# Kernel tuning notes

Measured on AMD Instinct MI355X. Metric: run time of the kernel, lower is better.

Reference implementation:

```python
import jax, jax.numpy as jnp
import numpy as np

B, S, HS, HHS, NH = 128, 8000, 9, 8, 4
HD = HHS // NH  # head dim = 2


def _layernorm(x, g, b, eps=1e-6):
    m = jnp.mean(x, axis=-1, keepdims=True)
    v = jnp.mean((x - m) ** 2, axis=-1, keepdims=True)
    return (x - m) * jax.lax.rsqrt(v + eps) * g + b


def _binding(a, b):
    # HRR binding: circular convolution along last dim
    return jnp.fft.ifft(jnp.fft.fft(a) * jnp.fft.fft(b)).real


def _unbinding(s, a):
    # HRR unbinding: circular correlation along last dim
    return jnp.fft.ifft(jnp.fft.fft(s) * jnp.conj(jnp.fft.fft(a))).real


def _cosine_sim(a, b, eps=1e-8):
    num = jnp.sum(a * b, axis=-1, keepdims=True)
    na = jnp.maximum(jnp.linalg.norm(a, axis=-1, keepdims=True), eps)
    nb = jnp.maximum(jnp.linalg.norm(b, axis=-1, keepdims=True), eps)
    return num / (na * nb)


def _heads(x):  # [B,S,HHS] -> [B,NH,S,HD]
    return x.reshape(B, S, NH, HD).transpose(0, 2, 1, 3)


def setup_inputs() -> dict:
    key = jax.random.key(0)
    ks = jax.random.split(key, 12)
    p = {}
    p["x"] = jax.random.normal(ks[0], (B, S, HS), dtype=jnp.float32)
    p["mask"] = jnp.ones((B, NH, S, 1), dtype=jnp.float32)
    p["pos_bias"] = jax.random.normal(ks[1], (1, S, HS), dtype=jnp.float32) * 0.02
    p["ln_g"] = jnp.ones((HS,), dtype=jnp.float32)
    p["ln_b"] = jnp.zeros((HS,), dtype=jnp.float32)
    p["Wq"] = jax.random.normal(ks[2], (HHS, HS), dtype=jnp.float32) * 0.3
    p["bq"] = jnp.zeros((HHS,), dtype=jnp.float32)
    p["Wk"] = jax.random.normal(ks[3], (HHS, HS), dtype=jnp.float32) * 0.3
    p["bk"] = jnp.zeros((HHS,), dtype=jnp.float32)
    p["Wv"] = jax.random.normal(ks[4], (HHS, HS), dtype=jnp.float32) * 0.3
    p["bv"] = jnp.zeros((HHS,), dtype=jnp.float32)
    p["W1"] = jax.random.normal(ks[5], (HS, HHS), dtype=jnp.float32) * 0.3
    p["b1"] = jnp.zeros((HS,), dtype=jnp.float32)
    p["W2"] = jax.random.normal(ks[6], (HS, HHS), dtype=jnp.float32) * 0.3
    p["b2"] = jnp.zeros((HS,), dtype=jnp.float32)
    p["Wo"] = jax.random.normal(ks[7], (1, HS), dtype=jnp.float32) * 0.3
    p["bo"] = jnp.zeros((1,), dtype=jnp.float32)
    return p


def reference(x, mask, pos_bias, ln_g, ln_b, Wq, bq, Wk, bk, Wv, bv, W1, b1, W2, b2, Wo, bo):
    x = x + pos_bias
    x = _layernorm(x, ln_g, ln_b)
    q = _heads(x @ Wq.T + bq)  # [B,NH,S,HD]
    k = _heads(x @ Wk.T + bk)
    v = _heads(x @ Wv.T + bv)
    bind = _binding(k, v).sum(axis=-2, keepdims=True)  # [B,NH,1,HD]
    vp = _unbinding(bind, q)                            # [B,NH,S,HD]
    scale = _cosine_sim(v, vp)                          # [B,NH,S,1]
    scale = scale + (1.0 - mask) * -1e9
    weight = jax.nn.softmax(scale, axis=-2)             # softmax over S
    weighted = weight * v                               # [B,NH,S,HD]
    attn_out = weighted.transpose(0, 2, 1, 3).reshape(B, S, HHS)
    # NOTE: original has dead code h=ffn1(attn_out); h=layernorm(h+x)
    # which is immediately overwritten and does not affect the output.
    h = jax.nn.gelu(attn_out @ W2.T + b2, approximate=False) + x
    return h @ Wo.T + bo  # [B,S,1]
```

## Files before the change

### kernel.cpp

```cpp
#include <hip/hip_runtime.h>
#include <math.h>

#define TB 256
#define S_LEN 8000
#define B_N 128
#define BPB 8
#define TPB 4
#define GRID (B_N * BPB)
#define CTRW 32


__device__ __forceinline__ void matvec89(const float* __restrict__ W, const float* __restrict__ bias,
                                         const float* __restrict__ y, float* out) {
#pragma unroll
  for (int i = 0; i < 8; ++i) {
    float a = bias[i];
#pragma unroll
    for (int j = 0; j < 9; ++j) a += W[i * 9 + j] * y[j];
    out[i] = a;
  }
}

__device__ __forceinline__ float head_scale(const float* q, const float* v, const float* bindS,
                                            int h, float maskv) {
  float q0 = q[2 * h], q1 = q[2 * h + 1];
  float v0 = v[2 * h], v1 = v[2 * h + 1];
  float B0 = bindS[2 * h], B1 = bindS[2 * h + 1];
  float vp0 = B0 * q0 + B1 * q1;
  float vp1 = B0 * q1 + B1 * q0;
  float num = v0 * vp0 + v1 * vp1;
  float a2 = fmaxf(v0 * v0 + v1 * v1, 1e-16f);
  float b2 = fmaxf(vp0 * vp0 + vp1 * vp1, 1e-16f);
  float sc = num * rsqrtf(a2 * b2);
  sc += (1.f - maskv) * (-1e9f);
  return sc;
}

__device__ __forceinline__ void batch_barrier(unsigned* ctr, int tid) {
  __syncthreads();
  if (tid == 0) {
    __hip_atomic_fetch_add(ctr, 1u, __ATOMIC_RELAXED, __HIP_MEMORY_SCOPE_AGENT);
    while (__hip_atomic_load(ctr, __ATOMIC_RELAXED, __HIP_MEMORY_SCOPE_AGENT) < (unsigned)BPB)
      __builtin_amdgcn_s_sleep(8);
  }
  __syncthreads();
}

__global__ void k_init(unsigned* __restrict__ ctrs, float* __restrict__ gws,
                       const float* __restrict__ W2, const float* __restrict__ b2,
                       const float* __restrict__ Wo, const float* __restrict__ bo) {
  int tid = blockIdx.x * blockDim.x + threadIdx.x;
  if (tid < 2 * B_N * CTRW) ctrs[tid] = 0u;
  if (blockIdx.x == 0 && threadIdx.x == 0) {
    float G[8];
#pragma unroll
    for (int j = 0; j < 8; ++j) G[j] = 0.f;
    float C0 = bo[0];
#pragma unroll
    for (int i = 0; i < 9; ++i) {
      float b = b2[i];
      float Phi = 0.5f * (1.f + erff(b * 0.70710678118654752f));
      float phi = 0.39894228040143268f * __expf(-0.5f * b * b);
      C0 += Wo[i] * (b * Phi);
      float wg = Wo[i] * (Phi + b * phi);
#pragma unroll
      for (int j = 0; j < 8; ++j) G[j] += wg * W2[i * 8 + j];
    }
#pragma unroll
    for (int j = 0; j < 8; ++j) gws[j] = G[j];
    gws[8] = C0;
  }
}

__global__ __launch_bounds__(TB, 4) void k_fused(
    const float* __restrict__ x, const float* __restrict__ mask, const float* __restrict__ pos,
    const float* __restrict__ lng, const float* __restrict__ lnb,
    const float* __restrict__ Wq, const float* __restrict__ bq,
    const float* __restrict__ Wk, const float* __restrict__ bk,
    const float* __restrict__ Wv, const float* __restrict__ bv,
    const float* __restrict__ Wo,
    const float* __restrict__ gws,
    unsigned* __restrict__ ctr1, unsigned* __restrict__ ctr2,
    float* __restrict__ bindP, float* __restrict__ sumP,
    float* __restrict__ out) {
  __shared__ float red[4 * 8];
  __shared__ float sib[BPB * 8];
  __shared__ float bindS[8], invDS[4];

  const int tid = threadIdx.x, bid = blockIdx.x;
  const int b = bid >> 3;
  const int t0 = (bid & 7) * TPB;
  const int wave = tid >> 6, lane = tid & 63;
  const float* maskb = mask + (size_t)b * 4 * S_LEN;

  int nrowA[TPB];
#pragma unroll
  for (int t = 0; t < TPB; ++t) nrowA[t] = min(TB, S_LEN - (t0 + t) * TB);

  float y[TPB][9];
  float vv[TPB][8];
  float acc[8];
#pragma unroll
  for (int i = 0; i < 8; ++i) acc[i] = 0.f;

#pragma unroll
  for (int t = 0; t < TPB; ++t) {
    if (tid < nrowA[t]) {
      const int s = (t0 + t) * TB + tid;
      const float* xr = x + ((size_t)b * S_LEN + s) * 9;
      const float* pr = pos + (size_t)s * 9;
      float m = 0.f;
#pragma unroll
      for (int j = 0; j < 9; ++j) { y[t][j] = xr[j] + pr[j]; m += y[t][j]; }
      m *= (1.f / 9.f);
      float var = 0.f;
#pragma unroll
      for (int j = 0; j < 9; ++j) { float d = y[t][j] - m; var += d * d; }
      var *= (1.f / 9.f);
      float rs = rsqrtf(var + 1e-6f);
#pragma unroll
      for (int j = 0; j < 9; ++j) y[t][j] = (y[t][j] - m) * rs * lng[j] + lnb[j];

      float kk[8];
      matvec89(Wk, bk, y[t], kk);
      matvec89(Wv, bv, y[t], vv[t]);
#pragma unroll
      for (int h = 0; h < 4; ++h) {
        float k0 = kk[2 * h], k1 = kk[2 * h + 1];
        float v0 = vv[t][2 * h], v1 = vv[t][2 * h + 1];
        acc[2 * h]     += k0 * v0 + k1 * v1;
        acc[2 * h + 1] += k0 * v1 + k1 * v0;
      }
    }
  }
#pragma unroll
  for (int i = 0; i < 8; ++i) {
#pragma unroll
    for (int off = 32; off > 0; off >>= 1) acc[i] += __shfl_down(acc[i], off, 64);
  }
  __syncthreads();
  if (lane == 0) {
#pragma unroll
    for (int i = 0; i < 8; ++i) red[wave * 8 + i] = acc[i];
  }
  __syncthreads();
  if (tid < 8) {
    float s = red[tid] + red[8 + tid] + red[16 + tid] + red[24 + tid];
    __hip_atomic_store(&bindP[bid * 8 + tid], s, __ATOMIC_RELAXED, __HIP_MEMORY_SCOPE_AGENT);
  }

  batch_barrier(&ctr1[b * CTRW], tid);

  if (tid < BPB * 8)
    sib[tid] = __hip_atomic_load(&bindP[(size_t)b * BPB * 8 + tid],
                                 __ATOMIC_RELAXED, __HIP_MEMORY_SCOPE_AGENT);
  __syncthreads();
  if (tid < 8) {
    float s = 0.f;
#pragma unroll
    for (int j = 0; j < BPB; ++j) s += sib[j * 8 + tid];
    bindS[tid] = s;
  }
  __syncthreads();

  float e[TPB][4];
  float gv[TPB][4];
  float oy[TPB];
  float esum[4] = {0.f, 0.f, 0.f, 0.f};
#pragma unroll
  for (int t = 0; t < TPB; ++t) {
    const int s0 = (t0 + t) * TB;
#pragma unroll
    for (int h = 0; h < 4; ++h) { e[t][h] = 0.f; gv[t][h] = 0.f; }
    oy[t] = 0.f;
    if (tid < nrowA[t]) {
      float qq[8];
      matvec89(Wq, bq, y[t], qq);
#pragma unroll
      for (int h = 0; h < 4; ++h) {
        float m = maskb[(size_t)h * S_LEN + s0 + tid];
        e[t][h] = __expf(head_scale(qq, vv[t], bindS, h, m));
        esum[h] += e[t][h];
        gv[t][h] = gws[2 * h] * vv[t][2 * h] + gws[2 * h + 1] * vv[t][2 * h + 1];
      }
      float o = 0.f;
#pragma unroll
      for (int i = 0; i < 9; ++i) o += Wo[i] * y[t][i];
      oy[t] = o;
    }
  }
#pragma unroll
  for (int h = 0; h < 4; ++h) {
#pragma unroll
    for (int off = 32; off > 0; off >>= 1) esum[h] += __shfl_down(esum[h], off, 64);
  }
  __syncthreads();
  if (lane == 0) {
#pragma unroll
    for (int h = 0; h < 4; ++h) red[wave * 4 + h] = esum[h];
  }
  __syncthreads();
  if (tid < 4) {
    float s = red[tid] + red[4 + tid] + red[8 + tid] + red[12 + tid];
    __hip_atomic_store(&sumP[bid * 4 + tid], s, __ATOMIC_RELAXED, __HIP_MEMORY_SCOPE_AGENT);
  }

  batch_barrier(&ctr2[b * CTRW], tid);

  if (tid < BPB * 4)
    sib[tid] = __hip_atomic_load(&sumP[(size_t)b * BPB * 4 + tid],
                                 __ATOMIC_RELAXED, __HIP_MEMORY_SCOPE_AGENT);
  __syncthreads();
  if (tid < 4) {
    float s = 0.f;
#pragma unroll
    for (int j = 0; j < BPB; ++j) s += sib[j * 4 + tid];
    invDS[tid] = 1.f / s;
  }
  __syncthreads();

  const float C0 = gws[8];
#pragma unroll
  for (int t = 0; t < TPB; ++t) {
    const int s0 = (t0 + t) * TB;
    if (tid < nrowA[t]) {
      float o = C0 + oy[t];
#pragma unroll
      for (int h = 0; h < 4; ++h) o += (e[t][h] * invDS[h]) * gv[t][h];
      out[(size_t)b * S_LEN + s0 + tid] = o;
    }
  }
}


extern "C" void kernel_launch(void* const* d_in, const int* in_sizes, int n_in,
                              void* d_out, int out_size, void* d_ws, size_t ws_size,
                              hipStream_t stream) {
  const float* x    = (const float*)d_in[0];
  const float* mask = (const float*)d_in[1];
  const float* pos  = (const float*)d_in[2];
  const float* lng  = (const float*)d_in[3];
  const float* lnb  = (const float*)d_in[4];
  const float* Wq   = (const float*)d_in[5];
  const float* bq   = (const float*)d_in[6];
  const float* Wk   = (const float*)d_in[7];
  const float* bk   = (const float*)d_in[8];
  const float* Wv   = (const float*)d_in[9];
  const float* bv   = (const float*)d_in[10];
  const float* W2   = (const float*)d_in[13];
  const float* b2   = (const float*)d_in[14];
  const float* Wo   = (const float*)d_in[15];
  const float* bo   = (const float*)d_in[16];
  float* out = (float*)d_out;

  unsigned* ctr1  = (unsigned*)d_ws;
  unsigned* ctr2  = ctr1 + B_N * CTRW;
  float*    gws   = (float*)(ctr2 + B_N * CTRW);
  float*    bindP = gws + 16;
  float*    sumP  = bindP + GRID * 8;

  k_init<<<(2 * B_N * CTRW + 255) / 256, 256, 0, stream>>>(ctr1, gws, W2, b2, Wo, bo);
  k_fused<<<GRID, TB, 0, stream>>>(x, mask, pos, lng, lnb, Wq, bq, Wk, bk, Wv, bv,
                                   Wo, gws, ctr1, ctr2, bindP, sumP, out);
}
```

Baseline: 32.08 us.

## Split first batch barrier into arrive/wait and overlap Q projection and mask loads

The first cross-block barrier becomes separate arrive and wait phases. Between them each block loads its mask values and computes the Q projection, the output projection term and the gate-weighted V term, so this work overlaps with waiting for the other blocks of the same batch. The spin-wait sleep interval also drops from 8 to 1. Keeping qq, mm and related values live across the barrier raises register pressure, which could reduce occupancy under the 4-blocks-per-SM launch bound.

```diff
diff --git a/kernel.cpp b/kernel.cpp
--- a/kernel.cpp
+++ b/kernel.cpp
@@ -41,7 +41,19 @@
   if (tid == 0) {
     __hip_atomic_fetch_add(ctr, 1u, __ATOMIC_RELAXED, __HIP_MEMORY_SCOPE_AGENT);
     while (__hip_atomic_load(ctr, __ATOMIC_RELAXED, __HIP_MEMORY_SCOPE_AGENT) < (unsigned)BPB)
-      __builtin_amdgcn_s_sleep(8);
+      __builtin_amdgcn_s_sleep(1);
+  }
+  __syncthreads();
+}
+__device__ __forceinline__ void barrier_arrive(unsigned* ctr, int tid) {
+  __syncthreads();
+  if (tid == 0)
+    __hip_atomic_fetch_add(ctr, 1u, __ATOMIC_RELAXED, __HIP_MEMORY_SCOPE_AGENT);
+}
+__device__ __forceinline__ void barrier_wait(unsigned* ctr, int tid) {
+  if (tid == 0) {
+    while (__hip_atomic_load(ctr, __ATOMIC_RELAXED, __HIP_MEMORY_SCOPE_AGENT) < (unsigned)BPB)
+      __builtin_amdgcn_s_sleep(1);
   }
   __syncthreads();
 }
@@ -149,7 +161,38 @@
     __hip_atomic_store(&bindP[bid * 8 + tid], s, __ATOMIC_RELAXED, __HIP_MEMORY_SCOPE_AGENT);
   }
 
-  batch_barrier(&ctr1[b * CTRW], tid);
+  barrier_arrive(&ctr1[b * CTRW], tid);
+
+  float mm[TPB][4];
+#pragma unroll
+  for (int t = 0; t < TPB; ++t) {
+    const int s = (t0 + t) * TB + tid;
+    if (tid < nrowA[t]) {
+#pragma unroll
+      for (int h = 0; h < 4; ++h) mm[t][h] = maskb[(size_t)h * S_LEN + s];
+    }
+  }
+  float qq[TPB][8];
+  float gv[TPB][4];
+  float oy[TPB];
+#pragma unroll
+  for (int t = 0; t < TPB; ++t) {
+#pragma unroll
+    for (int h = 0; h < 4; ++h) gv[t][h] = 0.f;
+    oy[t] = 0.f;
+    if (tid < nrowA[t]) {
+      matvec89(Wq, bq, y[t], qq[t]);
+      float o = 0.f;
+#pragma unroll
+      for (int i = 0; i < 9; ++i) o += Wo[i] * y[t][i];
+      oy[t] = o;
+#pragma unroll
+      for (int h = 0; h < 4; ++h)
+        gv[t][h] = gws[2 * h] * vv[t][2 * h] + gws[2 * h + 1] * vv[t][2 * h + 1];
+    }
+  }
+
+  barrier_wait(&ctr1[b * CTRW], tid);
 
   if (tid < BPB * 8)
     sib[tid] = __hip_atomic_load(&bindP[(size_t)b * BPB * 8 + tid],
@@ -164,29 +207,17 @@
   __syncthreads();
 
   float e[TPB][4];
-  float gv[TPB][4];
-  float oy[TPB];
   float esum[4] = {0.f, 0.f, 0.f, 0.f};
 #pragma unroll
   for (int t = 0; t < TPB; ++t) {
-    const int s0 = (t0 + t) * TB;
-#pragma unroll
-    for (int h = 0; h < 4; ++h) { e[t][h] = 0.f; gv[t][h] = 0.f; }
-    oy[t] = 0.f;
-    if (tid < nrowA[t]) {
-      float qq[8];
-      matvec89(Wq, bq, y[t], qq);
+#pragma unroll
+    for (int h = 0; h < 4; ++h) e[t][h] = 0.f;
+    if (tid < nrowA[t]) {
 #pragma unroll
       for (int h = 0; h < 4; ++h) {
-        float m = maskb[(size_t)h * S_LEN + s0 + tid];
-        e[t][h] = __expf(head_scale(qq, vv[t], bindS, h, m));
+        e[t][h] = __expf(head_scale(qq[t], vv[t], bindS, h, mm[t][h]));
         esum[h] += e[t][h];
-        gv[t][h] = gws[2 * h] * vv[t][2 * h] + gws[2 * h + 1] * vv[t][2 * h + 1];
       }
-      float o = 0.f;
-#pragma unroll
-      for (int i = 0; i < 9; ++i) o += Wo[i] * y[t][i];
-      oy[t] = o;
     }
   }
 #pragma unroll
```

Result: faster. 30.72 us (-4.3%).
